# Kernel tuning notes

Measured on AMD Instinct MI355X. Metric: run time of the kernel, lower is better.

The kernel has to match this reference:

```python
import jax, jax.numpy as jnp
import numpy as np

N = 8192
IN_F = 512
OUT_F = 256


def setup_inputs() -> dict:
    key = jax.random.key(0)
    k_x, k_adj, k_w, k_phi = jax.random.split(key, 4)
    x = jax.random.normal(k_x, (N, IN_F), dtype=jnp.float32)
    adj = jax.random.randint(k_adj, (N, N), 0, 2, dtype=jnp.int32)
    stdv_w = 1.0 / np.sqrt(OUT_F)
    weight = jax.random.uniform(k_w, (IN_F, OUT_F), minval=-stdv_w, maxval=stdv_w, dtype=jnp.float32)
    bias = jnp.zeros((OUT_F,), dtype=jnp.float32)
    stdv_p = 1.0  # 1/sqrt(phi.size(1)) = 1/sqrt(1)
    phi = jax.random.uniform(k_phi, (2 * OUT_F, 1), minval=-stdv_p, maxval=stdv_p, dtype=jnp.float32)
    return {"x": x, "adj": adj, "weight": weight, "bias": bias, "phi": phi}


def reference(x, adj, weight, bias, phi):
    # H = X W + b                                   [N, F]
    H = jnp.matmul(x, weight) + bias
    F_out = weight.shape[1]
    # Additive attention score: S[i,j] = [H_i ; H_j] . phi = H_i.phi_src + H_j.phi_dst
    # (H_interleaved indexes rows i, H_expanded indexes cols j in the torch code)
    s_src = jnp.matmul(H, phi[:F_out, 0])           # [N]
    s_dst = jnp.matmul(H, phi[F_out:, 0])           # [N]
    S = s_src[:, None] + s_dst[None, :]             # [N, N]
    n = x.shape[0]
    mask = (adj.astype(jnp.float32) + jnp.eye(n, dtype=jnp.float32)) != 0
    S_masked = jnp.where(mask, S, -jnp.inf)
    A = jax.nn.softmax(S_masked, axis=1)            # [N, N]
    return jnp.matmul(A, H)                         # [N, F]
```

## Files before the change

### kernel.cpp

```cpp
#include <hip/hip_runtime.h>
#include <hip/hip_bf16.h>
#include <stdint.h>

#define N_NODES 8192
#define IN_F 512
#define OUT_F 256

typedef __attribute__((ext_vector_type(8))) short bf16x8;
typedef __attribute__((ext_vector_type(4))) float f32x4;

__device__ __forceinline__ unsigned short f2bf_rn(float f) {
  union { float f; unsigned u; } v; v.f = f;
  unsigned r = v.u + 0x7FFFu + ((v.u >> 16) & 1u);
  return (unsigned short)(r >> 16);
}
__device__ __forceinline__ float bf2f(unsigned short h) {
  union { unsigned u; float f; } v; v.u = ((unsigned)h) << 16;
  return v.f;
}

__global__ __launch_bounds__(256) void k0_prep_w(const float* __restrict__ W,
                                                 short* __restrict__ Wh,
                                                 short* __restrict__ Wl) {
  int k = blockIdx.x;
  int c = threadIdx.x;
  float v = W[(size_t)k * OUT_F + c];
  unsigned short h = f2bf_rn(v);
  unsigned short l = f2bf_rn(v - bf2f(h));
  Wh[(size_t)c * IN_F + k] = (short)h;
  Wl[(size_t)c * IN_F + k] = (short)l;
}

__global__ __launch_bounds__(256) void k1_gemm_h(
    const float* __restrict__ X, const short* __restrict__ Wh,
    const short* __restrict__ Wl, const float* __restrict__ bias,
    float* __restrict__ H) {
  __shared__ __align__(16) short Xh[64 * 64], Xl[64 * 64];
  __shared__ __align__(16) short Wsh[128 * 64], Wsl[128 * 64];
  const int tid = threadIdx.x;
  const int rb = blockIdx.x >> 1, cb = blockIdx.x & 1;
  const int r0 = rb * 64, c0 = cb * 128;
  const int lane = tid & 63, wid = tid >> 6;

  f32x4 acc[8];
#pragma unroll
  for (int i = 0; i < 8; ++i) acc[i] = (f32x4){0.f, 0.f, 0.f, 0.f};

  const int sr = tid >> 2;
  const int sk = (tid & 3) * 16;

  for (int kc = 0; kc < IN_F; kc += 64) {
    const float* xp = X + (size_t)(r0 + sr) * IN_F + kc + sk;
#pragma unroll
    for (int q = 0; q < 2; ++q) {
      f32x4 v0 = *(const f32x4*)(xp + q * 8);
      f32x4 v1 = *(const f32x4*)(xp + q * 8 + 4);
      bf16x8 hv, lv;
#pragma unroll
      for (int j = 0; j < 4; ++j) {
        unsigned short h0 = f2bf_rn(v0[j]);
        hv[j] = (short)h0; lv[j] = (short)f2bf_rn(v0[j] - bf2f(h0));
        unsigned short h1 = f2bf_rn(v1[j]);
        hv[4 + j] = (short)h1; lv[4 + j] = (short)f2bf_rn(v1[j] - bf2f(h1));
      }
      int kb = (sk >> 3) + q;
      int off = sr * 64 + ((kb ^ (sr & 7)) << 3);
      *(bf16x8*)(Xh + off) = hv;
      *(bf16x8*)(Xl + off) = lv;
    }
#pragma unroll
    for (int it = 0; it < 4; ++it) {
      int u = it * 256 + tid;
      int col = u >> 3, kb = u & 7;
      size_t goff = (size_t)(c0 + col) * IN_F + kc + kb * 8;
      int off = col * 64 + ((kb ^ (col & 7)) << 3);
      *(bf16x8*)(Wsh + off) = *(const bf16x8*)(Wh + goff);
      *(bf16x8*)(Wsl + off) = *(const bf16x8*)(Wl + goff);
    }
    __syncthreads();
    const int arow = wid * 16 + (lane & 15);
    const int khalf = lane >> 4;
#pragma unroll
    for (int ks = 0; ks < 2; ++ks) {
      int kb = ks * 4 + khalf;
      int aoff = arow * 64 + ((kb ^ (arow & 7)) << 3);
      bf16x8 ah = *(const bf16x8*)(Xh + aoff);
      bf16x8 al = *(const bf16x8*)(Xl + aoff);
#pragma unroll
      for (int n = 0; n < 8; ++n) {
        int col = n * 16 + (lane & 15);
        int boff = col * 64 + ((kb ^ (col & 7)) << 3);
        bf16x8 bh = *(const bf16x8*)(Wsh + boff);
        bf16x8 bl = *(const bf16x8*)(Wsl + boff);
        acc[n] = __builtin_amdgcn_mfma_f32_16x16x32_bf16(ah, bh, acc[n], 0, 0, 0);
        acc[n] = __builtin_amdgcn_mfma_f32_16x16x32_bf16(ah, bl, acc[n], 0, 0, 0);
        acc[n] = __builtin_amdgcn_mfma_f32_16x16x32_bf16(al, bh, acc[n], 0, 0, 0);
      }
    }
    __syncthreads();
  }
  const int orow = r0 + wid * 16 + ((lane >> 4) << 2);
#pragma unroll
  for (int n = 0; n < 8; ++n) {
    int col = c0 + n * 16 + (lane & 15);
    float b = bias[col];
#pragma unroll
    for (int r = 0; r < 4; ++r)
      H[(size_t)(orow + r) * OUT_F + col] = acc[n][r] + b;
  }
}

__global__ __launch_bounds__(256) void k2_sdst(const float* __restrict__ H,
                                               const float* __restrict__ phi,
                                               float* __restrict__ sdst) {
  const int tid = threadIdx.x, lane = tid & 63, wid = tid >> 6;
  const int row = blockIdx.x * 4 + wid;
  f32x4 hv = *(const f32x4*)(H + (size_t)row * OUT_F + lane * 4);
  f32x4 pv = *(const f32x4*)(phi + OUT_F + lane * 4);
  float s = hv[0] * pv[0] + hv[1] * pv[1] + hv[2] * pv[2] + hv[3] * pv[3];
#pragma unroll
  for (int off = 32; off; off >>= 1) s += __shfl_xor(s, off);
  if (lane == 0) sdst[row] = s;
}

__global__ __launch_bounds__(1024) void k3_maxexp(const float* __restrict__ sdst,
                                                  float* __restrict__ e) {
  __shared__ float red[16];
  const int tid = threadIdx.x;
  float m = -1e30f;
  for (int j = tid; j < N_NODES; j += 1024) m = fmaxf(m, sdst[j]);
#pragma unroll
  for (int off = 32; off; off >>= 1) m = fmaxf(m, __shfl_xor(m, off));
  if ((tid & 63) == 0) red[tid >> 6] = m;
  __syncthreads();
  float gm = red[0];
#pragma unroll
  for (int i = 1; i < 16; ++i) gm = fmaxf(gm, red[i]);
  for (int j = tid; j < N_NODES; j += 1024) e[j] = expf(sdst[j] - gm);
}

__global__ __launch_bounds__(256) void k4_build_b(const float* __restrict__ H,
                                                  const float* __restrict__ e,
                                                  short* __restrict__ Bh,
                                                  short* __restrict__ Bl) {
  __shared__ float t[64][65];
  const int tid = threadIdx.x;
  const int tx = tid & 63, ty = tid >> 6;
  const int j0 = (blockIdx.x >> 2) * 64;
  const int c0 = (blockIdx.x & 3) * 64;
#pragma unroll
  for (int i = 0; i < 16; ++i) {
    int r = ty + i * 4;
    t[r][tx] = H[(size_t)(j0 + r) * OUT_F + c0 + tx];
  }
  __syncthreads();
  const float ej = e[j0 + tx];
#pragma unroll
  for (int i = 0; i < 16; ++i) {
    int c = c0 + ty + i * 4;
    float v = ej * t[tx][ty + i * 4];
    unsigned short h = f2bf_rn(v);
    unsigned short l = f2bf_rn(v - bf2f(h));
    Bh[(size_t)c * N_NODES + j0 + tx] = (short)h;
    Bl[(size_t)c * N_NODES + j0 + tx] = (short)l;
  }
}

__global__ __launch_bounds__(512) void k5_main(
    const int* __restrict__ adj, const short* __restrict__ Bh,
    const short* __restrict__ Bl, const float* __restrict__ e,
    float* __restrict__ part, float* __restrict__ dpartg, int kchunk) {
  __shared__ __align__(16) short Alds[128 * 64];
  __shared__ __align__(16) short Bhl[256 * 64];
  __shared__ __align__(16) short Bll[256 * 64];

  const int tid = threadIdx.x;
  const int rb = blockIdx.x & 63;
  const int ksi = blockIdx.x >> 6;
  const int r0 = rb * 128;
  const long kbeg = (long)ksi * kchunk;
  const int lane = tid & 63, wid = tid >> 6;

  f32x4 acc[16];
#pragma unroll
  for (int i = 0; i < 16; ++i) acc[i] = (f32x4){0.f, 0.f, 0.f, 0.f};

  const int sr = tid >> 2;
  const int sk = (tid & 3) * 16;
  const int irow = r0 + sr;
  float dsum = 0.f;

  for (long kc = kbeg; kc < kbeg + kchunk; kc += 64) {
    const int* ap = adj + (size_t)irow * N_NODES + kc + sk;
    const float* ep = e + kc + sk;
#pragma unroll
    for (int q = 0; q < 2; ++q) {
      int4 i0 = *(const int4*)(ap + q * 8);
      int4 i1 = *(const int4*)(ap + q * 8 + 4);
      f32x4 e0 = *(const f32x4*)(ep + q * 8);
      f32x4 e1 = *(const f32x4*)(ep + q * 8 + 4);
      long kg = kc + sk + q * 8;
      int vals[8] = {i0.x, i0.y, i0.z, i0.w, i1.x, i1.y, i1.z, i1.w};
      bf16x8 mv;
#pragma unroll
      for (int j = 0; j < 8; ++j) {
        bool m = (vals[j] != 0) || (kg + j == irow);
        mv[j] = m ? (short)0x3F80 : (short)0;
        float ej = (j < 4) ? e0[j] : e1[j - 4];
        dsum += m ? ej : 0.f;
      }
      int kb = (sk >> 3) + q;
      int off = sr * 64 + ((kb ^ (sr & 7)) << 3);
      *(bf16x8*)(Alds + off) = mv;
    }
#pragma unroll
    for (int it = 0; it < 4; ++it) {
      int u = it * 512 + tid;
      int col = u >> 3, kb = u & 7;
      size_t goff = (size_t)col * N_NODES + kc + kb * 8;
      int off = col * 64 + ((kb ^ (col & 7)) << 3);
      *(bf16x8*)(Bhl + off) = *(const bf16x8*)(Bh + goff);
      *(bf16x8*)(Bll + off) = *(const bf16x8*)(Bl + goff);
    }
    __syncthreads();
    const int arow = wid * 16 + (lane & 15);
    const int khalf = lane >> 4;
#pragma unroll
    for (int ks = 0; ks < 2; ++ks) {
      int kb = ks * 4 + khalf;
      int aoff = arow * 64 + ((kb ^ (arow & 7)) << 3);
      bf16x8 a = *(const bf16x8*)(Alds + aoff);
#pragma unroll
      for (int n = 0; n < 16; ++n) {
        int col = n * 16 + (lane & 15);
        int boff = col * 64 + ((kb ^ (col & 7)) << 3);
        bf16x8 bh = *(const bf16x8*)(Bhl + boff);
        bf16x8 bl = *(const bf16x8*)(Bll + boff);
        acc[n] = __builtin_amdgcn_mfma_f32_16x16x32_bf16(a, bh, acc[n], 0, 0, 0);
        acc[n] = __builtin_amdgcn_mfma_f32_16x16x32_bf16(a, bl, acc[n], 0, 0, 0);
      }
    }
    __syncthreads();
  }
  dsum += __shfl_xor(dsum, 1);
  dsum += __shfl_xor(dsum, 2);
  if ((tid & 3) == 0) dpartg[(size_t)ksi * N_NODES + irow] = dsum;
  const int orow0 = r0 + wid * 16 + ((lane >> 4) << 2);
  float* pbase = part + (size_t)ksi * N_NODES * OUT_F;
#pragma unroll
  for (int n = 0; n < 16; ++n) {
    int col = n * 16 + (lane & 15);
#pragma unroll
    for (int r = 0; r < 4; ++r)
      pbase[(size_t)(orow0 + r) * OUT_F + col] = acc[n][r];
  }
}

__global__ __launch_bounds__(256) void k6_final(const float* __restrict__ part,
                                                const float* __restrict__ dpart,
                                                float* __restrict__ out, int ksplit) {
  const int i = blockIdx.x, f = threadIdx.x;
  float num = 0.f, den = 0.f;
  for (int p = 0; p < ksplit; ++p) {
    num += part[((size_t)p * N_NODES + i) * OUT_F + f];
    den += dpart[(size_t)p * N_NODES + i];
  }
  out[(size_t)i * OUT_F + f] = num / den;
}

extern "C" void kernel_launch(void* const* d_in, const int* in_sizes, int n_in,
                              void* d_out, int out_size, void* d_ws, size_t ws_size,
                              hipStream_t stream) {
  const float* x    = (const float*)d_in[0];
  const int*   adj  = (const int*)d_in[1];
  const float* w    = (const float*)d_in[2];
  const float* bias = (const float*)d_in[3];
  const float* phi  = (const float*)d_in[4];
  float* out = (float*)d_out;
  char* ws = (char*)d_ws;

  size_t off = 0;
  auto alloc = [&](size_t bytes) {
    size_t o = off; off += (bytes + 255) & ~(size_t)255; return o;
  };
  size_t oH  = alloc((size_t)N_NODES * OUT_F * 4);
  size_t oWh = alloc((size_t)OUT_F * IN_F * 2);
  size_t oWl = alloc((size_t)OUT_F * IN_F * 2);
  size_t oSd = alloc((size_t)N_NODES * 4);
  size_t oE  = alloc((size_t)N_NODES * 4);
  size_t oBh = alloc((size_t)OUT_F * N_NODES * 2);
  size_t oBl = alloc((size_t)OUT_F * N_NODES * 2);
  int ksplit = 4;
  while (ksplit > 1 &&
         off + (size_t)ksplit * ((size_t)N_NODES * OUT_F * 4 + N_NODES * 4 + 512) > ws_size)
    ksplit >>= 1;
  size_t oPart = alloc((size_t)ksplit * N_NODES * OUT_F * 4);
  size_t oDp   = alloc((size_t)ksplit * N_NODES * 4);

  float* H  = (float*)(ws + oH);
  short* Wh = (short*)(ws + oWh);
  short* Wl = (short*)(ws + oWl);
  float* Sd = (float*)(ws + oSd);
  float* E  = (float*)(ws + oE);
  short* Bh = (short*)(ws + oBh);
  short* Bl = (short*)(ws + oBl);
  float* Part = (float*)(ws + oPart);
  float* Dp   = (float*)(ws + oDp);

  k0_prep_w<<<IN_F, OUT_F, 0, stream>>>(w, Wh, Wl);
  k1_gemm_h<<<256, 256, 0, stream>>>(x, Wh, Wl, bias, H);
  k2_sdst<<<N_NODES / 4, 256, 0, stream>>>(H, phi, Sd);
  k3_maxexp<<<1, 1024, 0, stream>>>(Sd, E);
  k4_build_b<<<512, 256, 0, stream>>>(H, E, Bh, Bl);
  k5_main<<<64 * ksplit, 512, 0, stream>>>(adj, Bh, Bl, E, Part, Dp, N_NODES / ksplit);
  k6_final<<<N_NODES, 256, 0, stream>>>(Part, Dp, out, ksplit);
}
```

Baseline: 546.6 us.

## Double-buffer main attention GEMM with async LDS loads and byte-packed adjacency

The main aggregation kernel is restructured. B tiles are now double-buffered through direct global-to-LDS loads, so the next tile's adjacency and B loads overlap the current tile's MFMAs. The adjacency mask is packed to bytes in LDS and expanded to bf16 at compute time. Warps now use a 4x4 MFMA tile grid instead of one row strip over all columns, which cuts LDS reads per MFMA. Separately, the single-block max/exp kernel is folded into the score and B-build kernels via per-block maxima, the B hi/lo planes are merged into one pre-swizzled buffer, and the self-loop term moves into the final reduction. The packing and the dsum arithmetic assume adjacency entries are exactly 0 or 1.

Result: faster. 483.0 us (-11.6%).

```diff
diff --git a/kernel.cpp b/kernel.cpp
--- a/kernel.cpp
+++ b/kernel.cpp
@@ -5,6 +5,7 @@
 #define N_NODES 8192
 #define IN_F 512
 #define OUT_F 256
+#define KSPLIT 4
 
 typedef __attribute__((ext_vector_type(8))) short bf16x8;
 typedef __attribute__((ext_vector_type(4))) float f32x4;
@@ -17,6 +18,23 @@
 __device__ __forceinline__ float bf2f(unsigned short h) {
   union { unsigned u; float f; } v; v.u = ((unsigned)h) << 16;
   return v.f;
+}
+
+__device__ __forceinline__ void gload_lds16(const void* g, void* l) {
+  __builtin_amdgcn_global_load_lds(
+      (const __attribute__((address_space(1))) unsigned int*)g,
+      (__attribute__((address_space(3))) unsigned int*)l, 16, 0, 0);
+}
+
+__device__ __forceinline__ bf16x8 expand8(uint2 b) {
+  unsigned c0 = b.x, c1 = b.x >> 16, c2 = b.y, c3 = b.y >> 16;
+  uint4 q;
+  q.x = ((c0 & 1u) | ((c0 & 0x100u) << 8)) * 0x3F80u;
+  q.y = ((c1 & 1u) | ((c1 & 0x100u) << 8)) * 0x3F80u;
+  q.z = ((c2 & 1u) | ((c2 & 0x100u) << 8)) * 0x3F80u;
+  q.w = ((c3 & 1u) | ((c3 & 0x100u) << 8)) * 0x3F80u;
+  union { uint4 u; bf16x8 v; } r; r.u = q;
+  return r.v;
 }
 
 __global__ __launch_bounds__(256) void k0_prep_w(const float* __restrict__ W,
@@ -112,7 +130,9 @@
 
 __global__ __launch_bounds__(256) void k2_sdst(const float* __restrict__ H,
                                                const float* __restrict__ phi,
-                                               float* __restrict__ sdst) {
+                                               float* __restrict__ sdst,
+                                               float* __restrict__ blockmax) {
+  __shared__ float r4[4];
   const int tid = threadIdx.x, lane = tid & 63, wid = tid >> 6;
   const int row = blockIdx.x * 4 + wid;
   f32x4 hv = *(const f32x4*)(H + (size_t)row * OUT_F + lane * 4);
@@ -120,150 +140,200 @@
   float s = hv[0] * pv[0] + hv[1] * pv[1] + hv[2] * pv[2] + hv[3] * pv[3];
 #pragma unroll
   for (int off = 32; off; off >>= 1) s += __shfl_xor(s, off);
-  if (lane == 0) sdst[row] = s;
-}
-
-__global__ __launch_bounds__(1024) void k3_maxexp(const float* __restrict__ sdst,
-                                                  float* __restrict__ e) {
-  __shared__ float red[16];
+  if (lane == 0) { sdst[row] = s; r4[wid] = s; }
+  __syncthreads();
+  if (tid == 0)
+    blockmax[blockIdx.x] = fmaxf(fmaxf(r4[0], r4[1]), fmaxf(r4[2], r4[3]));
+}
+
+__global__ __launch_bounds__(256) void k4_build(const float* __restrict__ H,
+                                                const float* __restrict__ sdst,
+                                                const float* __restrict__ blockmax,
+                                                short* __restrict__ Bs,
+                                                float* __restrict__ e) {
+  __shared__ float t[64][65];
+  __shared__ float red[4];
   const int tid = threadIdx.x;
   float m = -1e30f;
-  for (int j = tid; j < N_NODES; j += 1024) m = fmaxf(m, sdst[j]);
+  for (int i = tid; i < 2048; i += 256) m = fmaxf(m, blockmax[i]);
 #pragma unroll
   for (int off = 32; off; off >>= 1) m = fmaxf(m, __shfl_xor(m, off));
   if ((tid & 63) == 0) red[tid >> 6] = m;
   __syncthreads();
-  float gm = red[0];
-#pragma unroll
-  for (int i = 1; i < 16; ++i) gm = fmaxf(gm, red[i]);
-  for (int j = tid; j < N_NODES; j += 1024) e[j] = expf(sdst[j] - gm);
-}
-
-__global__ __launch_bounds__(256) void k4_build_b(const float* __restrict__ H,
-                                                  const float* __restrict__ e,
-                                                  short* __restrict__ Bh,
-                                                  short* __restrict__ Bl) {
-  __shared__ float t[64][65];
-  const int tid = threadIdx.x;
+  const float gmax = fmaxf(fmaxf(red[0], red[1]), fmaxf(red[2], red[3]));
+
   const int tx = tid & 63, ty = tid >> 6;
   const int j0 = (blockIdx.x >> 2) * 64;
   const int c0 = (blockIdx.x & 3) * 64;
 #pragma unroll
-  for (int i = 0; i < 16; ++i) {
-    int r = ty + i * 4;
-    t[r][tx] = H[(size_t)(j0 + r) * OUT_F + c0 + tx];
-  }
+  for (int i = 0; i < 16; ++i)
+    t[ty + i * 4][tx] = H[(size_t)(j0 + ty + i * 4) * OUT_F + c0 + tx];
   __syncthreads();
-  const float ej = e[j0 + tx];
+  const float ej = expf(sdst[j0 + tx] - gmax);
 #pragma unroll
   for (int i = 0; i < 16; ++i) {
     int c = c0 + ty + i * 4;
     float v = ej * t[tx][ty + i * 4];
     unsigned short h = f2bf_rn(v);
     unsigned short l = f2bf_rn(v - bf2f(h));
-    Bh[(size_t)c * N_NODES + j0 + tx] = (short)h;
-    Bl[(size_t)c * N_NODES + j0 + tx] = (short)l;
-  }
+    size_t kidx = (size_t)j0 + (tx ^ ((c & 7) << 3));
+    Bs[(size_t)c * N_NODES + kidx] = (short)h;
+    Bs[(size_t)(256 + c) * N_NODES + kidx] = (short)l;
+  }
+  if (c0 == 0 && tid < 64) e[j0 + tid] = expf(sdst[j0 + tid] - gmax);
 }
 
 __global__ __launch_bounds__(512) void k5_main(
-    const int* __restrict__ adj, const short* __restrict__ Bh,
-    const short* __restrict__ Bl, const float* __restrict__ e,
-    float* __restrict__ part, float* __restrict__ dpartg, int kchunk) {
-  __shared__ __align__(16) short Alds[128 * 64];
-  __shared__ __align__(16) short Bhl[256 * 64];
-  __shared__ __align__(16) short Bll[256 * 64];
+    const int* __restrict__ adj, const short* __restrict__ Bs,
+    const float* __restrict__ e, float* __restrict__ part,
+    float* __restrict__ dpartg, int kchunk) {
+  __shared__ __align__(16) unsigned char Ab[2][128 * 64];
+  __shared__ __align__(16) short Bb[2][2 * 256 * 64];
 
   const int tid = threadIdx.x;
-  const int rb = blockIdx.x & 63;
-  const int ksi = blockIdx.x >> 6;
+  const int bid = (int)(blockIdx.x & 7) * 32 + (int)(blockIdx.x >> 3);
+  const int rb = bid & 63, ksi = bid >> 6;
   const int r0 = rb * 128;
   const long kbeg = (long)ksi * kchunk;
   const int lane = tid & 63, wid = tid >> 6;
-
-  f32x4 acc[16];
-#pragma unroll
-  for (int i = 0; i < 16; ++i) acc[i] = (f32x4){0.f, 0.f, 0.f, 0.f};
+  const int wr = wid >> 2, wc = wid & 3;
+
+  f32x4 acc[4][4];
+#pragma unroll
+  for (int mi = 0; mi < 4; ++mi)
+#pragma unroll
+    for (int ni = 0; ni < 4; ++ni) acc[mi][ni] = (f32x4){0.f, 0.f, 0.f, 0.f};
 
   const int sr = tid >> 2;
-  const int sk = (tid & 3) * 16;
+  const int skq = tid & 3;
+  const int sk = skq * 16;
   const int irow = r0 + sr;
   float dsum = 0.f;
 
-  for (long kc = kbeg; kc < kbeg + kchunk; kc += 64) {
+  int4 a0, a1, a2, a3;
+  f32x4 ev0, ev1, ev2, ev3;
+
+  auto issueA = [&](long kc) {
     const int* ap = adj + (size_t)irow * N_NODES + kc + sk;
+    a0 = ((const int4*)ap)[0]; a1 = ((const int4*)ap)[1];
+    a2 = ((const int4*)ap)[2]; a3 = ((const int4*)ap)[3];
     const float* ep = e + kc + sk;
-#pragma unroll
-    for (int q = 0; q < 2; ++q) {
-      int4 i0 = *(const int4*)(ap + q * 8);
-      int4 i1 = *(const int4*)(ap + q * 8 + 4);
-      f32x4 e0 = *(const f32x4*)(ep + q * 8);
-      f32x4 e1 = *(const f32x4*)(ep + q * 8 + 4);
-      long kg = kc + sk + q * 8;
-      int vals[8] = {i0.x, i0.y, i0.z, i0.w, i1.x, i1.y, i1.z, i1.w};
-      bf16x8 mv;
-#pragma unroll
-      for (int j = 0; j < 8; ++j) {
-        bool m = (vals[j] != 0) || (kg + j == irow);
-        mv[j] = m ? (short)0x3F80 : (short)0;
-        float ej = (j < 4) ? e0[j] : e1[j - 4];
-        dsum += m ? ej : 0.f;
+    ev0 = ((const f32x4*)ep)[0]; ev1 = ((const f32x4*)ep)[1];
+    ev2 = ((const f32x4*)ep)[2]; ev3 = ((const f32x4*)ep)[3];
+  };
+  auto issueB = [&](long kc, int buf) {
+    const int p = wid >> 2;
+    const int cg = wid & 3;
+    const short* base = Bs + (size_t)p * 256 * N_NODES + kc;
+#pragma unroll
+    for (int i = 0; i < 8; ++i) {
+      int col = cg * 64 + i * 8 + (lane >> 3);
+      const short* g = base + (size_t)col * N_NODES + (lane & 7) * 8;
+      short* l = &Bb[buf][(p * 256 + cg * 64 + i * 8) * 64];
+      gload_lds16(g, l);
+    }
+  };
+  auto finishA = [&](int buf) {
+    dsum += (float)a0.x * ev0[0] + (float)a0.y * ev0[1] +
+            (float)a0.z * ev0[2] + (float)a0.w * ev0[3];
+    dsum += (float)a1.x * ev1[0] + (float)a1.y * ev1[1] +
+            (float)a1.z * ev1[2] + (float)a1.w * ev1[3];
+    dsum += (float)a2.x * ev2[0] + (float)a2.y * ev2[1] +
+            (float)a2.z * ev2[2] + (float)a2.w * ev2[3];
+    dsum += (float)a3.x * ev3[0] + (float)a3.y * ev3[1] +
+            (float)a3.z * ev3[2] + (float)a3.w * ev3[3];
+    unsigned u0 = (unsigned)a0.x | ((unsigned)a0.y << 8) |
+                  ((unsigned)a0.z << 16) | ((unsigned)a0.w << 24);
+    unsigned u1 = (unsigned)a1.x | ((unsigned)a1.y << 8) |
+                  ((unsigned)a1.z << 16) | ((unsigned)a1.w << 24);
+    unsigned u2 = (unsigned)a2.x | ((unsigned)a2.y << 8) |
+                  ((unsigned)a2.z << 16) | ((unsigned)a2.w << 24);
+    unsigned u3 = (unsigned)a3.x | ((unsigned)a3.y << 8) |
+                  ((unsigned)a3.z << 16) | ((unsigned)a3.w << 24);
+    const int g0 = skq * 2, g1 = g0 + 1;
+    uint2 w0; w0.x = u0; w0.y = u1;
+    uint2 w1; w1.x = u2; w1.y = u3;
+    *(uint2*)&Ab[buf][sr * 64 + ((g0 ^ (sr & 7)) << 3)] = w0;
+    *(uint2*)&Ab[buf][sr * 64 + ((g1 ^ (sr & 7)) << 3)] = w1;
+  };
+  auto compute = [&](int buf) {
+#pragma unroll
+    for (int ks = 0; ks < 2; ++ks) {
+      const int kb = ks * 4 + (lane >> 4);
+      bf16x8 af[4];
+#pragma unroll
+      for (int mi = 0; mi < 4; ++mi) {
+        int row = wr * 64 + mi * 16 + (lane & 15);
+        uint2 b = *(const uint2*)&Ab[buf][row * 64 + ((kb ^ (row & 7)) << 3)];
+        af[mi] = expand8(b);
       }
-      int kb = (sk >> 3) + q;
-      int off = sr * 64 + ((kb ^ (sr & 7)) << 3);
-      *(bf16x8*)(Alds + off) = mv;
-    }
-#pragma unroll
-    for (int it = 0; it < 4; ++it) {
-      int u = it * 512 + tid;
-      int col = u >> 3, kb = u & 7;
-      size_t goff = (size_t)col * N_NODES + kc + kb * 8;
-      int off = col * 64 + ((kb ^ (col & 7)) << 3);
-      *(bf16x8*)(Bhl + off) = *(const bf16x8*)(Bh + goff);
-      *(bf16x8*)(Bll + off) = *(const bf16x8*)(Bl + goff);
-    }
+#pragma unroll
+      for (int ni = 0; ni < 4; ++ni) {
+        int col = wc * 64 + ni * 16 + (lane & 15);
+        int so = (kb ^ (col & 7)) << 3;
+        bf16x8 bh = *(const bf16x8*)&Bb[buf][col * 64 + so];
+        bf16x8 bl = *(const bf16x8*)&Bb[buf][(256 + col) * 64 + so];
+#pragma unroll
+        for (int mi = 0; mi < 4; ++mi) {
+          acc[mi][ni] = __builtin_amdgcn_mfma_f32_16x16x32_bf16(af[mi], bh, acc[mi][ni], 0, 0, 0);
+          acc[mi][ni] = __builtin_amdgcn_mfma_f32_16x16x32_bf16(af[mi], bl, acc[mi][ni], 0, 0, 0);
+        }
+      }
+    }
+  };
+
+  issueA(kbeg); issueB(kbeg, 0); finishA(0);
+  __syncthreads();
+
+  const int NT = kchunk >> 6;
+  for (int t = 0; t < NT; ++t) {
+    const int cur = t & 1;
+    if (t + 1 < NT) {
+      const long kc = kbeg + (long)(t + 1) * 64;
+      issueA(kc);
+      issueB(kc, cur ^ 1);
+    }
+    compute(cur);
+    if (t + 1 < NT) finishA(cur ^ 1);
     __syncthreads();
-    const int arow = wid * 16 + (lane & 15);
-    const int khalf = lane >> 4;
-#pragma unroll
-    for (int ks = 0; ks < 2; ++ks) {
-      int kb = ks * 4 + khalf;
-      int aoff = arow * 64 + ((kb ^ (arow & 7)) << 3);
-      bf16x8 a = *(const bf16x8*)(Alds + aoff);
-#pragma unroll
-      for (int n = 0; n < 16; ++n) {
-        int col = n * 16 + (lane & 15);
-        int boff = col * 64 + ((kb ^ (col & 7)) << 3);
-        bf16x8 bh = *(const bf16x8*)(Bhl + boff);
-        bf16x8 bl = *(const bf16x8*)(Bll + boff);
-        acc[n] = __builtin_amdgcn_mfma_f32_16x16x32_bf16(a, bh, acc[n], 0, 0, 0);
-        acc[n] = __builtin_amdgcn_mfma_f32_16x16x32_bf16(a, bl, acc[n], 0, 0, 0);
-      }
-    }
-    __syncthreads();
-  }
+  }
+
   dsum += __shfl_xor(dsum, 1);
   dsum += __shfl_xor(dsum, 2);
   if ((tid & 3) == 0) dpartg[(size_t)ksi * N_NODES + irow] = dsum;
-  const int orow0 = r0 + wid * 16 + ((lane >> 4) << 2);
+
   float* pbase = part + (size_t)ksi * N_NODES * OUT_F;
-#pragma unroll
-  for (int n = 0; n < 16; ++n) {
-    int col = n * 16 + (lane & 15);
-#pragma unroll
-    for (int r = 0; r < 4; ++r)
-      pbase[(size_t)(orow0 + r) * OUT_F + col] = acc[n][r];
+  const int orow0 = r0 + wr * 64 + ((lane >> 4) << 2);
+#pragma unroll
+  for (int mi = 0; mi < 4; ++mi) {
+    int orow = orow0 + mi * 16;
+#pragma unroll
+    for (int ni = 0; ni < 4; ++ni) {
+      int col = wc * 64 + ni * 16 + (lane & 15);
+#pragma unroll
+      for (int r = 0; r < 4; ++r)
+        pbase[(size_t)(orow + r) * OUT_F + col] = acc[mi][ni][r];
+    }
   }
 }
 
 __global__ __launch_bounds__(256) void k6_final(const float* __restrict__ part,
                                                 const float* __restrict__ dpart,
-                                                float* __restrict__ out, int ksplit) {
+                                                const float* __restrict__ H,
+                                                const float* __restrict__ e,
+                                                const int* __restrict__ adj,
+                                                float* __restrict__ out) {
   const int i = blockIdx.x, f = threadIdx.x;
   float num = 0.f, den = 0.f;
-  for (int p = 0; p < ksplit; ++p) {
+#pragma unroll
+  for (int p = 0; p < KSPLIT; ++p) {
     num += part[((size_t)p * N_NODES + i) * OUT_F + f];
     den += dpart[(size_t)p * N_NODES + i];
+  }
+  if (adj[(size_t)i * N_NODES + i] == 0) {
+    float ei = e[i];
+    num += ei * H[(size_t)i * OUT_F + f];
+    den += ei;
   }
   out[(size_t)i * OUT_F + f] = num / den;
 }
@@ -283,35 +353,31 @@
   auto alloc = [&](size_t bytes) {
     size_t o = off; off += (bytes + 255) & ~(size_t)255; return o;
   };
-  size_t oH  = alloc((size_t)N_NODES * OUT_F * 4);
-  size_t oWh = alloc((size_t)OUT_F * IN_F * 2);
-  size_t oWl = alloc((size_t)OUT_F * IN_F * 2);
-  size_t oSd = alloc((size_t)N_NODES * 4);
-  size_t oE  = alloc((size_t)N_NODES * 4);
-  size_t oBh = alloc((size_t)OUT_F * N_NODES * 2);
-  size_t oBl = alloc((size_t)OUT_F * N_NODES * 2);
-  int ksplit = 4;
-  while (ksplit > 1 &&
-         off + (size_t)ksplit * ((size_t)N_NODES * OUT_F * 4 + N_NODES * 4 + 512) > ws_size)
-    ksplit >>= 1;
-  size_t oPart = alloc((size_t)ksplit * N_NODES * OUT_F * 4);
-  size_t oDp   = alloc((size_t)ksplit * N_NODES * 4);
-
-  float* H  = (float*)(ws + oH);
-  short* Wh = (short*)(ws + oWh);
-  short* Wl = (short*)(ws + oWl);
-  float* Sd = (float*)(ws + oSd);
-  float* E  = (float*)(ws + oE);
-  short* Bh = (short*)(ws + oBh);
-  short* Bl = (short*)(ws + oBl);
+  size_t oH   = alloc((size_t)N_NODES * OUT_F * 4);
+  size_t oWh  = alloc((size_t)OUT_F * IN_F * 2);
+  size_t oWl  = alloc((size_t)OUT_F * IN_F * 2);
+  size_t oSd  = alloc((size_t)N_NODES * 4);
+  size_t oBm  = alloc((size_t)2048 * 4);
+  size_t oE   = alloc((size_t)N_NODES * 4);
+  size_t oBs  = alloc((size_t)2 * OUT_F * N_NODES * 2);
+  size_t oPart = alloc((size_t)KSPLIT * N_NODES * OUT_F * 4);
+  size_t oDp   = alloc((size_t)KSPLIT * N_NODES * 4);
+  (void)oDp; (void)ws_size;
+
+  float* H   = (float*)(ws + oH);
+  short* Wh  = (short*)(ws + oWh);
+  short* Wl  = (short*)(ws + oWl);
+  float* Sd  = (float*)(ws + oSd);
+  float* Bm  = (float*)(ws + oBm);
+  float* E   = (float*)(ws + oE);
+  short* Bs  = (short*)(ws + oBs);
   float* Part = (float*)(ws + oPart);
   float* Dp   = (float*)(ws + oDp);
 
   k0_prep_w<<<IN_F, OUT_F, 0, stream>>>(w, Wh, Wl);
   k1_gemm_h<<<256, 256, 0, stream>>>(x, Wh, Wl, bias, H);
-  k2_sdst<<<N_NODES / 4, 256, 0, stream>>>(H, phi, Sd);
-  k3_maxexp<<<1, 1024, 0, stream>>>(Sd, E);
-  k4_build_b<<<512, 256, 0, stream>>>(H, E, Bh, Bl);
-  k5_main<<<64 * ksplit, 512, 0, stream>>>(adj, Bh, Bl, E, Part, Dp, N_NODES / ksplit);
-  k6_final<<<N_NODES, 256, 0, stream>>>(Part, Dp, out, ksplit);
-}
+  k2_sdst<<<N_NODES / 4, 256, 0, stream>>>(H, phi, Sd, Bm);
+  k4_build<<<512, 256, 0, stream>>>(H, Sd, Bm, Bs, E);
+  k5_main<<<64 * KSPLIT, 512, 0, stream>>>(adj, Bs, E, Part, Dp, N_NODES / KSPLIT);
+  k6_final<<<N_NODES, 256, 0, stream>>>(Part, Dp, H, E, adj, out);
+}
```
